# Performance work log

Hardware: AMD Instinct MI355X
Metric: run time of the kernel (lower is better)

Reference implementation:

```python
import jax, jax.numpy as jnp
import numpy as np

B, C, H, W = 8, 512, 64, 64
CH = C // 2          # channels per branch after chunk
R = CH // 4          # reduced channels (reduction=4)


def conv1x1(x, w, b):
    # x: [B,c,H,W], w: [o,c], b: [o]  (1x1 conv == per-pixel matmul)
    return jnp.einsum('oc,bchw->bohw', w, x) + b[None, :, None, None]


def spatial_self_corr(x, w1, b1, w2, b2, wo, bo):
    # DANet-style position attention. x: [B,CH,H,W]
    b_, c_, h_, w_ = x.shape
    n = h_ * w_
    q = conv1x1(x, w1, b1).reshape(b_, -1, n)   # [B,R,N]
    k = conv1x1(x, w2, b2).reshape(b_, -1, n)   # [B,R,N]
    attn = jax.nn.softmax(jnp.einsum('brn,brm->bnm', q, k), axis=-1)  # [B,N,N]
    out = jnp.einsum('brn,bnm->brm', k, attn)   # v = k (reduced channels), [B,R,N]
    out = out.reshape(b_, -1, h_, w_)
    return conv1x1(out, wo, bo)                 # [B,CH,H,W]


def channel_self_corr(x, wq, bq, wk, bk, wo, bo):
    # DANet-style channel attention over reduced channels. x: [B,CH,H,W]
    b_, c_, h_, w_ = x.shape
    n = h_ * w_
    q = conv1x1(x, wq, bq).reshape(b_, -1, n)   # [B,R,N]
    k = conv1x1(x, wk, bk).reshape(b_, -1, n)   # [B,R,N]
    attn = jax.nn.softmax(jnp.einsum('brn,bsn->brs', q, k), axis=-1)  # [B,R,R]
    out = jnp.einsum('brs,bsn->brn', attn, k)   # v = k (reduced channels)
    out = out.reshape(b_, -1, h_, w_)
    return conv1x1(out, wo, bo)                 # [B,CH,H,W]


def ckam_forward(top_feat, bottom_feat, wt, bt, wb, bb,
                 s_w1, s_b1, s_w2, s_b2, s_wo, s_bo,
                 c_wq, c_bq, c_wk, c_bk, c_wo, c_bo, f_w, f_b):
    top = conv1x1(top_feat, wt, bt)
    bottom = conv1x1(bottom_feat, wb, bb)
    x = top + bottom                            # [B,C,H,W]
    x1, x2 = jnp.split(x, 2, axis=1)            # each [B,C/2,H,W]
    ssc_out = spatial_self_corr(x1, s_w1, s_b1, s_w2, s_b2, s_wo, s_bo)
    csc_out = channel_self_corr(x2, c_wq, c_bq, c_wk, c_bk, c_wo, c_bo)
    out = jnp.concatenate([ssc_out, csc_out], axis=1)  # [B,C,H,W]
    return conv1x1(out, f_w, f_b)


def setup_inputs() -> dict:
    key = jax.random.key(0)
    ks = jax.random.split(key, 24)
    s = 0.02
    d = {
        'top_feat': jax.random.normal(ks[0], (B, C, H, W), jnp.float32),
        'bottom_feat': jax.random.normal(ks[1], (B, C, H, W), jnp.float32),
        'wt': jax.random.normal(ks[2], (C, C), jnp.float32) * s,
        'bt': jnp.zeros((C,), jnp.float32),
        'wb': jax.random.normal(ks[3], (C, C), jnp.float32) * s,
        'bb': jnp.zeros((C,), jnp.float32),
        's_w1': jax.random.normal(ks[4], (R, CH), jnp.float32) * s,
        's_b1': jnp.zeros((R,), jnp.float32),
        's_w2': jax.random.normal(ks[5], (R, CH), jnp.float32) * s,
        's_b2': jnp.zeros((R,), jnp.float32),
        's_wo': jax.random.normal(ks[6], (CH, R), jnp.float32) * s,
        's_bo': jnp.zeros((CH,), jnp.float32),
        'c_wq': jax.random.normal(ks[7], (R, CH), jnp.float32) * s,
        'c_bq': jnp.zeros((R,), jnp.float32),
        'c_wk': jax.random.normal(ks[8], (R, CH), jnp.float32) * s,
        'c_bk': jnp.zeros((R,), jnp.float32),
        'c_wo': jax.random.normal(ks[9], (CH, R), jnp.float32) * s,
        'c_bo': jnp.zeros((CH,), jnp.float32),
        'f_w': jax.random.normal(ks[10], (C, C), jnp.float32) * s,
        'f_b': jnp.zeros((C,), jnp.float32),
    }
    return d


def reference(top_feat, bottom_feat, wt, bt, wb, bb,
              s_w1, s_b1, s_w2, s_b2, s_wo, s_bo,
              c_wq, c_bq, c_wk, c_bk, c_wo, c_bo, f_w, f_b):
    return ckam_forward(top_feat, bottom_feat, wt, bt, wb, bb,
                        s_w1, s_b1, s_w2, s_b2, s_wo, s_bo,
                        c_wq, c_bq, c_wk, c_bk, c_wo, c_bo, f_w, f_b)
```

## Files before the change

### kernel.cpp

```cpp
#include <hip/hip_runtime.h>

typedef unsigned short u16;
typedef unsigned int   u32;
typedef __attribute__((ext_vector_type(8))) short short8;
typedef __attribute__((ext_vector_type(4))) float f32x4;

__device__ __forceinline__ u16 f2bf(float f) {
  u32 u = __float_as_uint(f);
  u32 r = u + 0x7fffu + ((u >> 16) & 1u);
  return (u16)(r >> 16);
}

__global__ __launch_bounds__(256) void k_combine_qk(
    const float* __restrict__ wt, const float* __restrict__ bt,
    const float* __restrict__ wb, const float* __restrict__ bb,
    const float* __restrict__ s_w1, const float* __restrict__ s_b1,
    const float* __restrict__ s_w2, const float* __restrict__ s_b2,
    const float* __restrict__ c_wq, const float* __restrict__ c_bq,
    const float* __restrict__ c_wk, const float* __restrict__ c_bk,
    u16* __restrict__ Wqkb, float* __restrict__ bqk) {
  int j = blockIdx.x;
  int g = j >> 6, r = j & 63;
  const float* sw; const float* sb;
  if (g == 0)      { sw = s_w1; sb = s_b1; }
  else if (g == 1) { sw = s_w2; sb = s_b2; }
  else if (g == 2) { sw = c_wq; sb = c_bq; }
  else             { sw = c_wk; sb = c_bk; }
  int cbase = (g < 2) ? 0 : 256;

  __shared__ float swr[256];
  __shared__ float red[256];
  int t = threadIdx.x;
  swr[t] = sw[r * 256 + t];
  __syncthreads();

  float a0 = 0.f, a1 = 0.f, a2 = 0.f, a3 = 0.f;
  for (int c = 0; c < 256; ++c) {
    float a = swr[c];
    int row = (cbase + c) * 512;
    a0 += a * wt[row + t];
    a1 += a * wt[row + 256 + t];
    a2 += a * wb[row + t];
    a3 += a * wb[row + 256 + t];
  }
  Wqkb[j * 1024 + t]       = f2bf(a0);
  Wqkb[j * 1024 + 256 + t] = f2bf(a1);
  Wqkb[j * 1024 + 512 + t] = f2bf(a2);
  Wqkb[j * 1024 + 768 + t] = f2bf(a3);

  red[t] = swr[t] * (bt[cbase + t] + bb[cbase + t]);
  __syncthreads();
  for (int s = 128; s > 0; s >>= 1) {
    if (t < s) red[t] += red[t + s];
    __syncthreads();
  }
  if (t == 0) bqk[j] = red[0] + sb[r];
}

__global__ __launch_bounds__(128) void k_combine_f(
    const float* __restrict__ f_w, const float* __restrict__ f_b,
    const float* __restrict__ s_wo, const float* __restrict__ s_bo,
    const float* __restrict__ c_wo, const float* __restrict__ c_bo,
    u16* __restrict__ Wfb, float* __restrict__ bfb) {
  int o = blockIdx.x;
  int t = threadIdx.x;
  __shared__ float fwr[512];
  __shared__ float red[128];
  for (int i = t; i < 512; i += 128) fwr[i] = f_w[o * 512 + i];
  __syncthreads();

  float acc = 0.f;
  if (t < 64) {
    for (int c = 0; c < 256; ++c) acc += fwr[c] * s_wo[c * 64 + t];
  } else {
    int rr = t - 64;
    for (int c = 0; c < 256; ++c) acc += fwr[256 + c] * c_wo[c * 64 + rr];
  }
  Wfb[o * 128 + t] = f2bf(acc);

  red[t] = fwr[t] * s_bo[t] + fwr[t + 128] * s_bo[t + 128]
         + fwr[256 + t] * c_bo[t] + fwr[384 + t] * c_bo[t + 128];
  __syncthreads();
  for (int s = 64; s > 0; s >>= 1) {
    if (t < s) red[t] += red[t + s];
    __syncthreads();
  }
  if (t == 0) bfb[o] = red[0] + f_b[o];
}

__global__ __launch_bounds__(256) void k_gemm_qk_mfma(
    const float* __restrict__ top, const float* __restrict__ bot,
    const u16* __restrict__ Wqkb, const float* __restrict__ bqk,
    float* __restrict__ qk) {
  int b = blockIdx.z, j0 = blockIdx.y * 128, n0 = blockIdx.x * 128;
  __shared__ u16 Aj[128][40];
  __shared__ u16 Xs[128][40];
  int t = threadIdx.x;
  int wv = t >> 6, lane = t & 63;
  int wr = wv >> 1, wc = wv & 1;
  int q = lane >> 4, l = lane & 15;

  f32x4 acc[4][4];
#pragma unroll
  for (int tr = 0; tr < 4; ++tr)
#pragma unroll
    for (int tc = 0; tc < 4; ++tc) acc[tr][tc] = (f32x4){0.f, 0.f, 0.f, 0.f};

  int xn = t & 31;
  int xs = t >> 5;

  for (int kc = 0; kc < 1024; kc += 32) {
    __syncthreads();
    {
      const u32* asrc = reinterpret_cast<const u32*>(Wqkb + (size_t)j0 * 1024 + kc);
#pragma unroll
      for (int p = 0; p < 8; ++p) {
        int i = p * 256 + t;
        int row = i >> 4, c = i & 15;
        *reinterpret_cast<u32*>(&Aj[row][c * 2]) = asrc[(size_t)row * 512 + c];
      }
    }
    const float* src = (kc < 512) ? top : bot;
    int c0 = (kc < 512) ? kc : kc - 512;
    const float* xb = src + (size_t)(b * 512 + c0) * 4096 + n0;
#pragma unroll
    for (int p = 0; p < 8; ++p) {
      int n = xn + 32 * (p >> 1);
      int kp = xs + 8 * (p & 1);
      float v0 = xb[(size_t)(2 * kp) * 4096 + n];
      float v1 = xb[(size_t)(2 * kp + 1) * 4096 + n];
      *reinterpret_cast<u32*>(&Xs[n][kp * 2]) =
          (u32)f2bf(v0) | ((u32)f2bf(v1) << 16);
    }
    __syncthreads();

    short8 af[4], bfr[4];
#pragma unroll
    for (int tr = 0; tr < 4; ++tr)
      af[tr] = *reinterpret_cast<const short8*>(&Aj[wr * 64 + tr * 16 + l][q * 8]);
#pragma unroll
    for (int tc = 0; tc < 4; ++tc)
      bfr[tc] = *reinterpret_cast<const short8*>(&Xs[wc * 64 + tc * 16 + l][q * 8]);
#pragma unroll
    for (int tr = 0; tr < 4; ++tr)
#pragma unroll
      for (int tc = 0; tc < 4; ++tc)
        acc[tr][tc] = __builtin_amdgcn_mfma_f32_16x16x32_bf16(
            af[tr], bfr[tc], acc[tr][tc], 0, 0, 0);
  }

#pragma unroll
  for (int tr = 0; tr < 4; ++tr) {
    int j = j0 + wr * 64 + tr * 16 + q * 4;
    float4 bias = *reinterpret_cast<const float4*>(&bqk[j]);
#pragma unroll
    for (int tc = 0; tc < 4; ++tc) {
      int n = n0 + wc * 64 + tc * 16 + l;
      float* dst = qk + (size_t)(b * 256 + j) * 4096 + n;
      dst[0]        = acc[tr][tc][0] + bias.x;
      dst[4096]     = acc[tr][tc][1] + bias.y;
      dst[2 * 4096] = acc[tr][tc][2] + bias.z;
      dst[3 * 4096] = acc[tr][tc][3] + bias.w;
    }
  }
}

__global__ __launch_bounds__(256) void k_transpose_qk(
    const float* __restrict__ qk, u16* __restrict__ q1t, u16* __restrict__ k1t) {
  int b = blockIdx.y, n0 = blockIdx.x * 64;
  __shared__ u16 T[128][68];
  int t = threadIdx.x;
  for (int i = t; i < 8192; i += 256) {
    int j = i >> 6, n = i & 63;
    T[j][n] = f2bf(qk[((size_t)(b * 256) + j) * 4096 + n0 + n]);
  }
  __syncthreads();
  int n = t & 63, h = t >> 6;
  u16 buf[32];
#pragma unroll
  for (int jj = 0; jj < 32; ++jj) buf[jj] = T[h * 32 + jj][n];
  u16* dst;
  if (h < 2) dst = q1t + ((size_t)(b * 4096) + n0 + n) * 64 + h * 32;
  else       dst = k1t + ((size_t)(b * 4096) + n0 + n) * 64 + (h - 2) * 32;
  u32* d32 = reinterpret_cast<u32*>(dst);
#pragma unroll
  for (int k = 0; k < 16; ++k)
    d32[k] = (u32)buf[2 * k] | ((u32)buf[2 * k + 1] << 16);
}

__global__ __launch_bounds__(256) void k_sp_stats_mfma(
    const u16* __restrict__ q1t, const u16* __restrict__ k1t,
    float* __restrict__ dinv) {
  int b = blockIdx.y, n0 = blockIdx.x * 64;
  __shared__ u16 Qs[64][72];
  __shared__ float red[4][64][16];
  int t = threadIdx.x;
  int wv = t >> 6, lane = t & 63;
  int q = lane >> 4, l = lane & 15;

  {
    const u32* src = reinterpret_cast<const u32*>(q1t + ((size_t)(b * 4096) + n0) * 64);
    for (int i = t; i < 2048; i += 256) {
      int n = i >> 5, c = i & 31;
      reinterpret_cast<u32*>(&Qs[n][0])[c] = src[n * 32 + c];
    }
  }
  __syncthreads();

  short8 afr[4][2];
#pragma unroll
  for (int tn = 0; tn < 4; ++tn)
#pragma unroll
    for (int kh = 0; kh < 2; ++kh)
      afr[tn][kh] = *reinterpret_cast<const short8*>(&Qs[tn * 16 + l][kh * 32 + q * 8]);

  const u16* kbase = k1t + (size_t)b * 4096 * 64;
  float dsum[4][4];
#pragma unroll
  for (int tn = 0; tn < 4; ++tn)
#pragma unroll
    for (int i = 0; i < 4; ++i) dsum[tn][i] = 0.f;

  for (int mt = wv; mt < 64; mt += 4) {
    int m0 = mt * 64;
#pragma unroll
    for (int tm = 0; tm < 4; ++tm) {
      const u16* kp = kbase + ((size_t)(m0 + tm * 16 + l)) * 64;
      short8 b0 = *reinterpret_cast<const short8*>(kp + q * 8);
      short8 b1 = *reinterpret_cast<const short8*>(kp + 32 + q * 8);
#pragma unroll
      for (int tn = 0; tn < 4; ++tn) {
        f32x4 acc = {0.f, 0.f, 0.f, 0.f};
        acc = __builtin_amdgcn_mfma_f32_16x16x32_bf16(afr[tn][0], b0, acc, 0, 0, 0);
        acc = __builtin_amdgcn_mfma_f32_16x16x32_bf16(afr[tn][1], b1, acc, 0, 0, 0);
#pragma unroll
        for (int i = 0; i < 4; ++i) dsum[tn][i] += __expf(acc[i]);
      }
    }
  }

#pragma unroll
  for (int tn = 0; tn < 4; ++tn)
#pragma unroll
    for (int i = 0; i < 4; ++i)
      red[wv][tn * 16 + q * 4 + i][l] = dsum[tn][i];
  __syncthreads();
  if (t < 64) {
    float s = 0.f;
#pragma unroll
    for (int v = 0; v < 4; ++v)
#pragma unroll
      for (int u = 0; u < 16; ++u) s += red[v][t][u];
    dinv[(size_t)b * 4096 + n0 + t] = 1.0f / s;
  }
}

__global__ __launch_bounds__(256) void k_scale_k1d(
    const float* __restrict__ qk, const float* __restrict__ dinv,
    u16* __restrict__ k1d) {
  int b = blockIdx.x >> 6, r = blockIdx.x & 63;
  const float* src = qk + ((size_t)(b * 256) + 64 + r) * 4096;
  const float* dv = dinv + (size_t)b * 4096;
  u16* dst = k1d + ((size_t)(b * 64) + r) * 4096;
  for (int i = threadIdx.x; i < 4096; i += 256)
    dst[i] = f2bf(src[i] * dv[i]);
}

#define NSPLIT 2

__device__ __forceinline__ void gl_lds16(const u16* g, u16* l) {
  __builtin_amdgcn_global_load_lds(
      (const __attribute__((address_space(1))) u32*)g,
      (__attribute__((address_space(3))) u32*)l, 16, 0, 0);
}

__device__ __forceinline__ void stage_qk(const u16* qb, const u16* kb, int noff,
                                         u16* qdst, u16* kdst,
                                         int wv, int rsub, int scol) {
#pragma unroll
  for (int pp = 0; pp < 2; ++pp) {
    int p = wv * 2 + pp;
    int row = p * 8 + rsub;
    gl_lds16(qb + ((size_t)(noff + row)) * 64 + scol * 8, qdst + p * 512);
    gl_lds16(kb + (size_t)row * 4096 + noff + scol * 8, kdst + p * 512);
  }
}

__global__ __launch_bounds__(256) void k_sp_apply_mfma(
    const u16* __restrict__ q1t, const u16* __restrict__ k1t,
    const u16* __restrict__ k1d, float* __restrict__ spre) {
  int b = blockIdx.z, m0 = blockIdx.x * 64;
  int n_base = blockIdx.y * (4096 / NSPLIT);
  const int NT = 64 / NSPLIT;

  __shared__ __align__(16) u16 Qs[2][64][64];
  __shared__ __align__(16) u16 Ks[2][64][64];
  __shared__ __align__(16) u16 Wt[64][64];

  int t = threadIdx.x;
  int wv = t >> 6, lane = t & 63;
  int q = lane >> 4, l = lane & 15;
  int sw = l & 7;
  int rsub = lane >> 3;
  int scol = (lane & 7) ^ rsub;

  const u16* ktp = k1t + ((size_t)(b * 4096) + m0 + wv * 16 + l) * 64;
  short8 bS0 = *reinterpret_cast<const short8*>(ktp + q * 8);
  short8 bS1 = *reinterpret_cast<const short8*>(ktp + 32 + q * 8);

  const u16* qb = q1t + (size_t)b * 4096 * 64;
  const u16* kb = k1d + (size_t)b * 64 * 4096;

  f32x4 accO[4];
#pragma unroll
  for (int tr = 0; tr < 4; ++tr) accO[tr] = (f32x4){0.f, 0.f, 0.f, 0.f};

  stage_qk(qb, kb, n_base, &Qs[0][0][0], &Ks[0][0][0], wv, rsub, scol);
  __syncthreads();

  int wrow = wv * 16 + l;
  char* wp = reinterpret_cast<char*>(&Wt[wrow][0]);
  int c_a0 = (q ^ sw) << 4;
  int c_a1 = c_a0 ^ 64;

  int cur = 0;
  for (int nt = 0; nt < NT; ++nt) {
    if (nt + 1 < NT)
      stage_qk(qb, kb, n_base + (nt + 1) * 64,
               &Qs[cur ^ 1][0][0], &Ks[cur ^ 1][0][0], wv, rsub, scol);

    const u16(*Qc)[64] = Qs[cur];
    const u16(*Kc)[64] = Ks[cur];

#pragma unroll
    for (int tn = 0; tn < 4; ++tn) {
      const char* qrow = reinterpret_cast<const char*>(&Qc[tn * 16 + l][0]);
      short8 a0 = *reinterpret_cast<const short8*>(qrow + c_a0);
      short8 a1 = *reinterpret_cast<const short8*>(qrow + c_a1);
      f32x4 s = {0.f, 0.f, 0.f, 0.f};
      s = __builtin_amdgcn_mfma_f32_16x16x32_bf16(a0, bS0, s, 0, 0, 0);
      s = __builtin_amdgcn_mfma_f32_16x16x32_bf16(a1, bS1, s, 0, 0, 0);
      u16 w0 = f2bf(__expf(s[0]));
      u16 w1 = f2bf(__expf(s[1]));
      u16 w2 = f2bf(__expf(s[2]));
      u16 w3 = f2bf(__expf(s[3]));
      uint2 pk;
      pk.x = (u32)w0 | ((u32)w1 << 16);
      pk.y = (u32)w2 | ((u32)w3 << 16);
      *reinterpret_cast<uint2*>(
          wp + ((((tn * 2 + (q >> 1)) ^ sw) << 4) | ((q & 1) << 3))) = pk;
    }

    short8 bW0 = *reinterpret_cast<const short8*>(wp + c_a0);
    short8 bW1 = *reinterpret_cast<const short8*>(wp + c_a1);
#pragma unroll
    for (int tr = 0; tr < 4; ++tr) {
      const char* krow = reinterpret_cast<const char*>(&Kc[tr * 16 + l][0]);
      short8 a0 = *reinterpret_cast<const short8*>(krow + c_a0);
      short8 a1 = *reinterpret_cast<const short8*>(krow + c_a1);
      accO[tr] = __builtin_amdgcn_mfma_f32_16x16x32_bf16(a0, bW0, accO[tr], 0, 0, 0);
      accO[tr] = __builtin_amdgcn_mfma_f32_16x16x32_bf16(a1, bW1, accO[tr], 0, 0, 0);
    }

    __syncthreads();
    cur ^= 1;
  }

#pragma unroll
  for (int tr = 0; tr < 4; ++tr)
#pragma unroll
    for (int i = 0; i < 4; ++i)
      atomicAdd(&spre[(size_t)(b * 64 + tr * 16 + q * 4 + i) * 4096 + m0 + wrow],
                accO[tr][i]);
}

__global__ __launch_bounds__(256) void k_ch_scores(
    const float* __restrict__ qk, float* __restrict__ part) {
  int b = blockIdx.y, ch = blockIdx.x;
  const float* q2 = qk + (size_t)(b * 256 + 128) * 4096;
  const float* k2 = qk + (size_t)(b * 256 + 192) * 4096;
  __shared__ float Qs[64][65];
  __shared__ float Ks[64][65];
  int t = threadIdx.x, ti = t >> 4, tj = t & 15;
  float acc[4][4] = {};

  for (int sub = 0; sub < 8; ++sub) {
    int n0 = ch * 512 + sub * 64;
    __syncthreads();
    for (int i = t; i < 4096; i += 256) {
      int r = i >> 6, n = i & 63;
      Qs[r][n] = q2[(size_t)r * 4096 + n0 + n];
      Ks[r][n] = k2[(size_t)r * 4096 + n0 + n];
    }
    __syncthreads();
#pragma unroll
    for (int n = 0; n < 64; ++n) {
      float qa[4], ka[4];
#pragma unroll
      for (int i = 0; i < 4; ++i) qa[i] = Qs[ti * 4 + i][n];
#pragma unroll
      for (int jx = 0; jx < 4; ++jx) ka[jx] = Ks[tj * 4 + jx][n];
#pragma unroll
      for (int i = 0; i < 4; ++i)
#pragma unroll
        for (int jx = 0; jx < 4; ++jx) acc[i][jx] += qa[i] * ka[jx];
    }
  }
#pragma unroll
  for (int i = 0; i < 4; ++i)
#pragma unroll
    for (int jx = 0; jx < 4; ++jx)
      part[(size_t)(b * 8 + ch) * 4096 + (ti * 4 + i) * 64 + tj * 4 + jx] = acc[i][jx];
}

__global__ __launch_bounds__(64) void k_ch_softmax(
    const float* __restrict__ part, float* __restrict__ attn2) {
  int b = blockIdx.x, r = threadIdx.x;
  float v[64];
  float mx = -1e30f;
#pragma unroll
  for (int s = 0; s < 64; ++s) {
    float sum = 0.f;
#pragma unroll
    for (int c = 0; c < 8; ++c)
      sum += part[(size_t)(b * 8 + c) * 4096 + r * 64 + s];
    v[s] = sum;
    mx = fmaxf(mx, sum);
  }
  float den = 0.f;
#pragma unroll
  for (int s = 0; s < 64; ++s) { v[s] = __expf(v[s] - mx); den += v[s]; }
  float inv = 1.0f / den;
#pragma unroll
  for (int s = 0; s < 64; ++s)
    attn2[(size_t)b * 4096 + r * 64 + s] = v[s] * inv;
}

__global__ __launch_bounds__(256) void k_ch_apply(
    const float* __restrict__ qk, const float* __restrict__ attn2,
    float* __restrict__ cpre) {
  int b = blockIdx.y;
  int n = blockIdx.x * 256 + threadIdx.x;
  const float* k2 = qk + (size_t)(b * 256 + 192) * 4096;
  __shared__ float As[64][64];
  int t = threadIdx.x;
  for (int i = t; i < 4096; i += 256) As[i >> 6][i & 63] = attn2[(size_t)b * 4096 + i];
  __syncthreads();

  float acc[64];
#pragma unroll
  for (int r = 0; r < 64; ++r) acc[r] = 0.f;
  for (int s4 = 0; s4 < 64; s4 += 4) {
    float kv0 = k2[(size_t)(s4 + 0) * 4096 + n];
    float kv1 = k2[(size_t)(s4 + 1) * 4096 + n];
    float kv2 = k2[(size_t)(s4 + 2) * 4096 + n];
    float kv3 = k2[(size_t)(s4 + 3) * 4096 + n];
#pragma unroll
    for (int r = 0; r < 64; ++r) {
      float4 w = *reinterpret_cast<const float4*>(&As[r][s4]);
      acc[r] += w.x * kv0 + w.y * kv1 + w.z * kv2 + w.w * kv3;
    }
  }
#pragma unroll
  for (int r = 0; r < 64; ++r)
    cpre[(size_t)(b * 64 + r) * 4096 + n] = acc[r];
}

__global__ __launch_bounds__(256) void k_final_mfma(
    const float* __restrict__ spre, const float* __restrict__ cpre,
    const u16* __restrict__ Wfb, const float* __restrict__ bfb,
    float* __restrict__ out) {
  int b = blockIdx.z, o0 = blockIdx.y * 128, n0 = blockIdx.x * 128;
  __shared__ u16 Aj[128][40];
  __shared__ u16 Xs[128][40];
  int t = threadIdx.x;
  int wv = t >> 6, lane = t & 63;
  int wr = wv >> 1, wc = wv & 1;
  int q = lane >> 4, l = lane & 15;

  f32x4 acc[4][4];
#pragma unroll
  for (int tr = 0; tr < 4; ++tr)
#pragma unroll
    for (int tc = 0; tc < 4; ++tc) acc[tr][tc] = (f32x4){0.f, 0.f, 0.f, 0.f};

  int xn = t & 31;
  int xs = t >> 5;

  for (int kc = 0; kc < 128; kc += 32) {
    __syncthreads();
    {
      const u32* asrc = reinterpret_cast<const u32*>(Wfb + (size_t)o0 * 128 + kc);
#pragma unroll
      for (int p = 0; p < 8; ++p) {
        int i = p * 256 + t;
        int row = i >> 4, c = i & 15;
        *reinterpret_cast<u32*>(&Aj[row][c * 2]) = asrc[(size_t)row * 64 + c];
      }
    }
    const float* src = (kc < 64) ? spre : cpre;
    int r0 = (kc < 64) ? kc : kc - 64;
    const float* xb = src + (size_t)(b * 64 + r0) * 4096 + n0;
#pragma unroll
    for (int p = 0; p < 8; ++p) {
      int n = xn + 32 * (p >> 1);
      int kp = xs + 8 * (p & 1);
      float v0 = xb[(size_t)(2 * kp) * 4096 + n];
      float v1 = xb[(size_t)(2 * kp + 1) * 4096 + n];
      *reinterpret_cast<u32*>(&Xs[n][kp * 2]) =
          (u32)f2bf(v0) | ((u32)f2bf(v1) << 16);
    }
    __syncthreads();

    short8 af[4], bfr[4];
#pragma unroll
    for (int tr = 0; tr < 4; ++tr)
      af[tr] = *reinterpret_cast<const short8*>(&Aj[wr * 64 + tr * 16 + l][q * 8]);
#pragma unroll
    for (int tc = 0; tc < 4; ++tc)
      bfr[tc] = *reinterpret_cast<const short8*>(&Xs[wc * 64 + tc * 16 + l][q * 8]);
#pragma unroll
    for (int tr = 0; tr < 4; ++tr)
#pragma unroll
      for (int tc = 0; tc < 4; ++tc)
        acc[tr][tc] = __builtin_amdgcn_mfma_f32_16x16x32_bf16(
            af[tr], bfr[tc], acc[tr][tc], 0, 0, 0);
  }

#pragma unroll
  for (int tr = 0; tr < 4; ++tr) {
    int o = o0 + wr * 64 + tr * 16 + q * 4;
    float4 bias = *reinterpret_cast<const float4*>(&bfb[o]);
#pragma unroll
    for (int tc = 0; tc < 4; ++tc) {
      int n = n0 + wc * 64 + tc * 16 + l;
      float* dst = out + (size_t)(b * 512 + o) * 4096 + n;
      dst[0]        = acc[tr][tc][0] + bias.x;
      dst[4096]     = acc[tr][tc][1] + bias.y;
      dst[2 * 4096] = acc[tr][tc][2] + bias.z;
      dst[3 * 4096] = acc[tr][tc][3] + bias.w;
    }
  }
}

extern "C" void kernel_launch(void* const* d_in, const int* in_sizes, int n_in,
                              void* d_out, int out_size, void* d_ws, size_t ws_size,
                              hipStream_t stream) {
  const float* top  = (const float*)d_in[0];
  const float* bot  = (const float*)d_in[1];
  const float* wt   = (const float*)d_in[2];
  const float* bt   = (const float*)d_in[3];
  const float* wb   = (const float*)d_in[4];
  const float* bb   = (const float*)d_in[5];
  const float* s_w1 = (const float*)d_in[6];
  const float* s_b1 = (const float*)d_in[7];
  const float* s_w2 = (const float*)d_in[8];
  const float* s_b2 = (const float*)d_in[9];
  const float* s_wo = (const float*)d_in[10];
  const float* s_bo = (const float*)d_in[11];
  const float* c_wq = (const float*)d_in[12];
  const float* c_bq = (const float*)d_in[13];
  const float* c_wk = (const float*)d_in[14];
  const float* c_bk = (const float*)d_in[15];
  const float* c_wo = (const float*)d_in[16];
  const float* c_bo = (const float*)d_in[17];
  const float* f_w  = (const float*)d_in[18];
  const float* f_b  = (const float*)d_in[19];
  float* out = (float*)d_out;

  char* ob = (char*)d_out;
  float* qk = (float*)ob;
  u16* q1t = (u16*)(ob + 33554432);
  u16* k1t = (u16*)(ob + 37748736);
  u16* k1d = (u16*)(ob + 41943040);

  char* ws = (char*)d_ws;
  float* dinv  = (float*)(ws + 0);
  float* part  = (float*)(ws + 131072);
  float* attn2 = (float*)(ws + 1179648);
  float* spre  = (float*)(ws + 1310720);
  float* cpre  = (float*)(ws + 9699328);
  u16*   Wqkb  = (u16*)  (ws + 18087936);
  float* bqk   = (float*)(ws + 18612224);
  u16*   Wfb   = (u16*)  (ws + 18613248);
  float* bfb   = (float*)(ws + 18744320);

  hipMemsetAsync(spre, 0, 8388608, stream);

  k_combine_qk<<<256, 256, 0, stream>>>(wt, bt, wb, bb, s_w1, s_b1, s_w2, s_b2,
                                        c_wq, c_bq, c_wk, c_bk, Wqkb, bqk);
  k_combine_f<<<512, 128, 0, stream>>>(f_w, f_b, s_wo, s_bo, c_wo, c_bo, Wfb, bfb);
  k_gemm_qk_mfma<<<dim3(32, 2, 8), 256, 0, stream>>>(top, bot, Wqkb, bqk, qk);
  k_transpose_qk<<<dim3(64, 8), 256, 0, stream>>>(qk, q1t, k1t);
  k_sp_stats_mfma<<<dim3(64, 8), 256, 0, stream>>>(q1t, k1t, dinv);
  k_ch_scores<<<dim3(8, 8), 256, 0, stream>>>(qk, part);
  k_ch_softmax<<<8, 64, 0, stream>>>(part, attn2);
  k_ch_apply<<<dim3(16, 8), 256, 0, stream>>>(qk, attn2, cpre);
  k_scale_k1d<<<512, 256, 0, stream>>>(qk, dinv, k1d);
  k_sp_apply_mfma<<<dim3(64, NSPLIT, 8), 256, 0, stream>>>(q1t, k1t, k1d, spre);
  k_final_mfma<<<dim3(32, 4, 8), 256, 0, stream>>>(spre, cpre, Wfb, bfb, out);
}
```

Before: 462.5 us.

## Double-buffer QK GEMM with swizzled LDS and widen channel-attention kernel grids

The QK projection GEMM now double-buffers its LDS tiles. The weight tile is loaded asynchronously with global_load_lds into an XOR-swizzled layout, and the next activation tile is prefetched into registers while the MFMAs run, which cuts the syncs per K step and hides load latency. The channel-attention path is split more finely: ch_scores uses 32 chunks instead of 8, softmax gets one wave per row with shuffle reductions, and ch_apply gives each thread 16 rows instead of 64 across more blocks. This raises occupancy on kernels that used only 64–128 blocks, at the cost of a larger partial buffer placed in spare output memory and extra reduction reads.

```diff
diff --git a/kernel.cpp b/kernel.cpp
--- a/kernel.cpp
+++ b/kernel.cpp
@@ -9,6 +9,12 @@
   u32 u = __float_as_uint(f);
   u32 r = u + 0x7fffu + ((u >> 16) & 1u);
   return (u16)(r >> 16);
+}
+
+__device__ __forceinline__ void gl_lds16(const u16* g, u16* l) {
+  __builtin_amdgcn_global_load_lds(
+      (const __attribute__((address_space(1))) u32*)g,
+      (__attribute__((address_space(3))) u32*)l, 16, 0, 0);
 }
 
 __global__ __launch_bounds__(256) void k_combine_qk(
@@ -35,6 +41,7 @@
   __syncthreads();
 
   float a0 = 0.f, a1 = 0.f, a2 = 0.f, a3 = 0.f;
+#pragma unroll 4
   for (int c = 0; c < 256; ++c) {
     float a = swr[c];
     int row = (cbase + c) * 512;
@@ -71,9 +78,11 @@
 
   float acc = 0.f;
   if (t < 64) {
+#pragma unroll 4
     for (int c = 0; c < 256; ++c) acc += fwr[c] * s_wo[c * 64 + t];
   } else {
     int rr = t - 64;
+#pragma unroll 4
     for (int c = 0; c < 256; ++c) acc += fwr[256 + c] * c_wo[c * 64 + rr];
   }
   Wfb[o * 128 + t] = f2bf(acc);
@@ -93,8 +102,8 @@
     const u16* __restrict__ Wqkb, const float* __restrict__ bqk,
     float* __restrict__ qk) {
   int b = blockIdx.z, j0 = blockIdx.y * 128, n0 = blockIdx.x * 128;
-  __shared__ u16 Aj[128][40];
-  __shared__ u16 Xs[128][40];
+  __shared__ __align__(16) u16 Aj[2][128][32];
+  __shared__ __align__(16) u16 Xs[2][128][32];
   int t = threadIdx.x;
   int wv = t >> 6, lane = t & 63;
   int wr = wv >> 1, wc = wv & 1;
@@ -108,45 +117,77 @@
 
   int xn = t & 31;
   int xs = t >> 5;
-
-  for (int kc = 0; kc < 1024; kc += 32) {
-    __syncthreads();
-    {
-      const u32* asrc = reinterpret_cast<const u32*>(Wqkb + (size_t)j0 * 1024 + kc);
-#pragma unroll
-      for (int p = 0; p < 8; ++p) {
-        int i = p * 256 + t;
-        int row = i >> 4, c = i & 15;
-        *reinterpret_cast<u32*>(&Aj[row][c * 2]) = asrc[(size_t)row * 512 + c];
-      }
-    }
+  int asrow = (lane >> 2);
+  int asc = (lane & 3) ^ ((lane >> 2) & 3);
+  int fsw = (q ^ (l & 3)) << 4;
+
+  float xv[16];
+
+  auto stageA = [&](int kc, u16* dst) {
+#pragma unroll
+    for (int p = 0; p < 2; ++p) {
+      int cI = wv * 2 + p;
+      int row = cI * 16 + asrow;
+      gl_lds16(Wqkb + (size_t)(j0 + row) * 1024 + kc + asc * 8, dst + cI * 512);
+    }
+  };
+  auto loadX = [&](int kc) {
     const float* src = (kc < 512) ? top : bot;
-    int c0 = (kc < 512) ? kc : kc - 512;
+    int c0 = kc & 511;
     const float* xb = src + (size_t)(b * 512 + c0) * 4096 + n0;
 #pragma unroll
     for (int p = 0; p < 8; ++p) {
       int n = xn + 32 * (p >> 1);
       int kp = xs + 8 * (p & 1);
-      float v0 = xb[(size_t)(2 * kp) * 4096 + n];
-      float v1 = xb[(size_t)(2 * kp + 1) * 4096 + n];
-      *reinterpret_cast<u32*>(&Xs[n][kp * 2]) =
-          (u32)f2bf(v0) | ((u32)f2bf(v1) << 16);
-    }
-    __syncthreads();
-
+      xv[2 * p]     = xb[(size_t)(2 * kp) * 4096 + n];
+      xv[2 * p + 1] = xb[(size_t)(2 * kp + 1) * 4096 + n];
+    }
+  };
+  auto writeX = [&](u16* dst) {
+    char* base = reinterpret_cast<char*>(dst);
+#pragma unroll
+    for (int p = 0; p < 8; ++p) {
+      int n = xn + 32 * (p >> 1);
+      int kp = xs + 8 * (p & 1);
+      u32 v = (u32)f2bf(xv[2 * p]) | ((u32)f2bf(xv[2 * p + 1]) << 16);
+      *reinterpret_cast<u32*>(
+          base + n * 64 + ((((kp >> 2) ^ (n & 3)) << 4) | ((kp & 3) << 2))) = v;
+    }
+  };
+
+  stageA(0, &Aj[0][0][0]);
+  loadX(0);
+  writeX(&Xs[0][0][0]);
+  __syncthreads();
+
+  int cur = 0;
+  for (int it = 0; it < 32; ++it) {
+    if (it + 1 < 32) {
+      stageA((it + 1) * 32, &Aj[cur ^ 1][0][0]);
+      loadX((it + 1) * 32);
+    }
+    const char* Ab = reinterpret_cast<const char*>(&Aj[cur][0][0]);
+    const char* Xb = reinterpret_cast<const char*>(&Xs[cur][0][0]);
     short8 af[4], bfr[4];
 #pragma unroll
-    for (int tr = 0; tr < 4; ++tr)
-      af[tr] = *reinterpret_cast<const short8*>(&Aj[wr * 64 + tr * 16 + l][q * 8]);
-#pragma unroll
-    for (int tc = 0; tc < 4; ++tc)
-      bfr[tc] = *reinterpret_cast<const short8*>(&Xs[wc * 64 + tc * 16 + l][q * 8]);
+    for (int tr = 0; tr < 4; ++tr) {
+      int row = wr * 64 + tr * 16 + l;
+      af[tr] = *reinterpret_cast<const short8*>(Ab + row * 64 + fsw);
+    }
+#pragma unroll
+    for (int tc = 0; tc < 4; ++tc) {
+      int row = wc * 64 + tc * 16 + l;
+      bfr[tc] = *reinterpret_cast<const short8*>(Xb + row * 64 + fsw);
+    }
 #pragma unroll
     for (int tr = 0; tr < 4; ++tr)
 #pragma unroll
       for (int tc = 0; tc < 4; ++tc)
         acc[tr][tc] = __builtin_amdgcn_mfma_f32_16x16x32_bf16(
             af[tr], bfr[tc], acc[tr][tc], 0, 0, 0);
+    if (it + 1 < 32) writeX(&Xs[cur ^ 1][0][0]);
+    __syncthreads();
+    cur ^= 1;
   }
 
 #pragma unroll
@@ -267,12 +308,6 @@
 }
 
 #define NSPLIT 2
-
-__device__ __forceinline__ void gl_lds16(const u16* g, u16* l) {
-  __builtin_amdgcn_global_load_lds(
-      (const __attribute__((address_space(1))) u32*)g,
-      (__attribute__((address_space(3))) u32*)l, 16, 0, 0);
-}
 
 __device__ __forceinline__ void stage_qk(const u16* qb, const u16* kb, int noff,
                                          u16* qdst, u16* kdst,
@@ -384,8 +419,8 @@
   int t = threadIdx.x, ti = t >> 4, tj = t & 15;
   float acc[4][4] = {};
 
-  for (int sub = 0; sub < 8; ++sub) {
-    int n0 = ch * 512 + sub * 64;
+  for (int sub = 0; sub < 2; ++sub) {
+    int n0 = ch * 128 + sub * 64;
     __syncthreads();
     for (int i = t; i < 4096; i += 256) {
       int r = i >> 6, n = i & 63;
@@ -410,60 +445,61 @@
   for (int i = 0; i < 4; ++i)
 #pragma unroll
     for (int jx = 0; jx < 4; ++jx)
-      part[(size_t)(b * 8 + ch) * 4096 + (ti * 4 + i) * 64 + tj * 4 + jx] = acc[i][jx];
+      part[(size_t)(b * 32 + ch) * 4096 + (ti * 4 + i) * 64 + tj * 4 + jx] = acc[i][jx];
 }
 
 __global__ __launch_bounds__(64) void k_ch_softmax(
     const float* __restrict__ part, float* __restrict__ attn2) {
-  int b = blockIdx.x, r = threadIdx.x;
-  float v[64];
-  float mx = -1e30f;
-#pragma unroll
-  for (int s = 0; s < 64; ++s) {
-    float sum = 0.f;
-#pragma unroll
-    for (int c = 0; c < 8; ++c)
-      sum += part[(size_t)(b * 8 + c) * 4096 + r * 64 + s];
-    v[s] = sum;
-    mx = fmaxf(mx, sum);
-  }
-  float den = 0.f;
-#pragma unroll
-  for (int s = 0; s < 64; ++s) { v[s] = __expf(v[s] - mx); den += v[s]; }
-  float inv = 1.0f / den;
-#pragma unroll
-  for (int s = 0; s < 64; ++s)
-    attn2[(size_t)b * 4096 + r * 64 + s] = v[s] * inv;
+  int bid = blockIdx.x;
+  int b = bid >> 6, r = bid & 63;
+  int s = threadIdx.x;
+  const float* p0 = part + (size_t)(b * 32) * 4096 + r * 64 + s;
+  float sum = 0.f;
+#pragma unroll
+  for (int c = 0; c < 32; ++c) sum += p0[(size_t)c * 4096];
+  float mx = sum;
+#pragma unroll
+  for (int o = 32; o > 0; o >>= 1) mx = fmaxf(mx, __shfl_xor(mx, o));
+  float e = __expf(sum - mx);
+  float den = e;
+#pragma unroll
+  for (int o = 32; o > 0; o >>= 1) den += __shfl_xor(den, o);
+  attn2[(size_t)b * 4096 + r * 64 + s] = e / den;
 }
 
 __global__ __launch_bounds__(256) void k_ch_apply(
     const float* __restrict__ qk, const float* __restrict__ attn2,
     float* __restrict__ cpre) {
   int b = blockIdx.y;
-  int n = blockIdx.x * 256 + threadIdx.x;
+  int t = threadIdx.x;
+  int n = blockIdx.x * 64 + (t & 63);
+  int qr = t >> 6;
   const float* k2 = qk + (size_t)(b * 256 + 192) * 4096;
   __shared__ float As[64][64];
-  int t = threadIdx.x;
-  for (int i = t; i < 4096; i += 256) As[i >> 6][i & 63] = attn2[(size_t)b * 4096 + i];
-  __syncthreads();
-
-  float acc[64];
-#pragma unroll
-  for (int r = 0; r < 64; ++r) acc[r] = 0.f;
+  {
+    float4* As4 = reinterpret_cast<float4*>(&As[0][0]);
+    const float4* a4 = reinterpret_cast<const float4*>(attn2 + (size_t)b * 4096);
+    for (int i = t; i < 1024; i += 256) As4[i] = a4[i];
+  }
+  __syncthreads();
+
+  float acc[16];
+#pragma unroll
+  for (int rr = 0; rr < 16; ++rr) acc[rr] = 0.f;
   for (int s4 = 0; s4 < 64; s4 += 4) {
     float kv0 = k2[(size_t)(s4 + 0) * 4096 + n];
     float kv1 = k2[(size_t)(s4 + 1) * 4096 + n];
     float kv2 = k2[(size_t)(s4 + 2) * 4096 + n];
     float kv3 = k2[(size_t)(s4 + 3) * 4096 + n];
 #pragma unroll
-    for (int r = 0; r < 64; ++r) {
-      float4 w = *reinterpret_cast<const float4*>(&As[r][s4]);
-      acc[r] += w.x * kv0 + w.y * kv1 + w.z * kv2 + w.w * kv3;
-    }
-  }
-#pragma unroll
-  for (int r = 0; r < 64; ++r)
-    cpre[(size_t)(b * 64 + r) * 4096 + n] = acc[r];
+    for (int rr = 0; rr < 16; ++rr) {
+      float4 w = *reinterpret_cast<const float4*>(&As[qr * 16 + rr][s4]);
+      acc[rr] += w.x * kv0 + w.y * kv1 + w.z * kv2 + w.w * kv3;
+    }
+  }
+#pragma unroll
+  for (int rr = 0; rr < 16; ++rr)
+    cpre[(size_t)(b * 64 + qr * 16 + rr) * 4096 + n] = acc[rr];
 }
 
 __global__ __launch_bounds__(256) void k_final_mfma(
@@ -573,10 +609,10 @@
   u16* q1t = (u16*)(ob + 33554432);
   u16* k1t = (u16*)(ob + 37748736);
   u16* k1d = (u16*)(ob + 41943040);
+  float* part = (float*)(ob + 46137344);
 
   char* ws = (char*)d_ws;
   float* dinv  = (float*)(ws + 0);
-  float* part  = (float*)(ws + 131072);
   float* attn2 = (float*)(ws + 1179648);
   float* spre  = (float*)(ws + 1310720);
   float* cpre  = (float*)(ws + 9699328);
@@ -593,9 +629,9 @@
   k_gemm_qk_mfma<<<dim3(32, 2, 8), 256, 0, stream>>>(top, bot, Wqkb, bqk, qk);
   k_transpose_qk<<<dim3(64, 8), 256, 0, stream>>>(qk, q1t, k1t);
   k_sp_stats_mfma<<<dim3(64, 8), 256, 0, stream>>>(q1t, k1t, dinv);
-  k_ch_scores<<<dim3(8, 8), 256, 0, stream>>>(qk, part);
-  k_ch_softmax<<<8, 64, 0, stream>>>(part, attn2);
-  k_ch_apply<<<dim3(16, 8), 256, 0, stream>>>(qk, attn2, cpre);
+  k_ch_scores<<<dim3(32, 8), 256, 0, stream>>>(qk, part);
+  k_ch_softmax<<<512, 64, 0, stream>>>(part, attn2);
+  k_ch_apply<<<dim3(64, 8), 256, 0, stream>>>(qk, attn2, cpre);
   k_scale_k1d<<<512, 256, 0, stream>>>(qk, dinv, k1d);
   k_sp_apply_mfma<<<dim3(64, NSPLIT, 8), 256, 0, stream>>>(q1t, k1t, k1d, spre);
   k_final_mfma<<<dim3(32, 4, 8), 256, 0, stream>>>(spre, cpre, Wfb, bfb, out);
```

After: 447.9 us. 1.03x faster.
